# Performance work log

Hardware: AMD Instinct MI355X
Metric: run time of the kernel (lower is better)

## Reference

```python
import jax, jax.numpy as jnp
import numpy as np

# Cyclic permutation matrices applied after each flow step (dimension==3 branch)
P_XY = jnp.array([[0, 1, 0], [1, 0, 0], [0, 0, 1]], dtype=jnp.float32)
P_XZ = jnp.array([[0, 0, 1], [0, 1, 0], [1, 0, 0]], dtype=jnp.float32)
P_YZ = jnp.array([[0, 1, 0], [0, 0, 1], [1, 0, 0]], dtype=jnp.float32)

N = 1_000_000   # number of atoms / samples
FLOW_DEPTH = 8


def setup_inputs() -> dict:
    key = jax.random.key(0)
    k1, k2, k3 = jax.random.split(key, 3)
    z = jax.random.normal(k1, (N, 3), dtype=jnp.float32)
    w = jax.random.normal(k2, (N, FLOW_DEPTH, 3, 3), dtype=jnp.float32)
    b = jax.random.normal(k3, (N, FLOW_DEPTH, 3), dtype=jnp.float32)
    return {"z": z, "w": w, "b": b}


def _flow_zx(z, w, b):
    # z: [N,3], w: [N,D,3,3], b: [N,D,3]
    eye = jnp.eye(3, dtype=w.dtype)
    diag = jnp.diagonal(w, axis1=-2, axis2=-1)               # [N,D,3]
    # LU parameterization: unit lower-tri L, positive diag D, unit upper-tri U
    l = jnp.tril(w, -1) + eye
    u = jnp.triu(w, 1) + eye
    # Faithful to original: log-det uses |0.1 + diag|, D uses |diag| + 0.1
    d_log_det = jnp.sum(jnp.log(jnp.abs(0.1 + diag)), axis=(1, 2))  # [N]
    du = (jnp.abs(diag) + 0.1)[..., :, None] * u             # D @ U, [N,D,3,3]
    W = jnp.einsum('ndij,ndjk->ndik', l, du)                  # L @ D @ U
    perms = [P_XY, P_YZ, P_XZ]
    depth = w.shape[1]
    for idx in range(depth):  # static, small flow depth
        z = jnp.einsum('nb,nbd->nd', z, W[:, idx]) + b[:, idx]
        z = z @ perms[idx % 3]
    return z, d_log_det


def reference(z, w, b):
    return _flow_zx(z, w, b)
```

## Files before the change

### kernel.cpp

```cpp
#include <hip/hip_runtime.h>

#define FLOW_DEPTH 8
#define BLOCK 64
#define W_F4 18
#define B_F4 6

typedef const __attribute__((address_space(1))) void g_void;
typedef __attribute__((address_space(3))) void l_void;

__global__ __launch_bounds__(BLOCK) void graphflow_kernel(
    const float* __restrict__ z_in,
    const float* __restrict__ w,
    const float* __restrict__ b,
    float* __restrict__ out,
    int n_atoms)
{
    __shared__ float4 sw[BLOCK * W_F4];
    __shared__ float4 sb[BLOCK * B_F4];

    const int t = threadIdx.x;
    const int atom0 = blockIdx.x * BLOCK;

    const float4* gw = reinterpret_cast<const float4*>(w) + (size_t)atom0 * W_F4;
    const float4* gb = reinterpret_cast<const float4*>(b) + (size_t)atom0 * B_F4;

    if (atom0 + BLOCK <= n_atoms) {
#pragma unroll
        for (int k = 0; k < W_F4; ++k) {
            __builtin_amdgcn_global_load_lds((g_void*)(gw + k * BLOCK + t),
                                             (l_void*)(sw + k * BLOCK), 16, 0, 0);
        }
#pragma unroll
        for (int k = 0; k < B_F4; ++k) {
            __builtin_amdgcn_global_load_lds((g_void*)(gb + k * BLOCK + t),
                                             (l_void*)(sb + k * BLOCK), 16, 0, 0);
        }
    } else {
        int nw = (n_atoms - atom0) * W_F4;
        for (int k = 0; k < W_F4; ++k) {
            int idx = k * BLOCK + t;
            if (idx < nw) sw[idx] = gw[idx];
        }
        int nb = (n_atoms - atom0) * B_F4;
        for (int k = 0; k < B_F4; ++k) {
            int idx = k * BLOCK + t;
            if (idx < nb) sb[idx] = gb[idx];
        }
    }

    __builtin_amdgcn_s_waitcnt(0);
    __syncthreads();

    const int n = atom0 + t;
    if (n >= n_atoms) return;

    float4 wr[W_F4];
#pragma unroll
    for (int j = 0; j < W_F4; ++j) wr[j] = sw[t * W_F4 + j];
    float4 br[B_F4];
#pragma unroll
    for (int j = 0; j < B_F4; ++j) br[j] = sb[t * B_F4 + j];

    const float* wf = reinterpret_cast<const float*>(wr);
    const float* bf = reinterpret_cast<const float*>(br);

    float z0 = z_in[n * 3 + 0];
    float z1 = z_in[n * 3 + 1];
    float z2 = z_in[n * 3 + 2];

    float logdet = 0.0f;

#pragma unroll
    for (int d = 0; d < FLOW_DEPTH; ++d) {
        const float* W = wf + d * 9;
        float w00 = W[0], w01 = W[1], w02 = W[2];
        float w10 = W[3], w11 = W[4], w12 = W[5];
        float w20 = W[6], w21 = W[7], w22 = W[8];

        float d0 = fabsf(w00) + 0.1f;
        float d1 = fabsf(w11) + 0.1f;
        float d2 = fabsf(w22) + 0.1f;
        logdet += logf(fabsf(0.1f + w00)) +
                  logf(fabsf(0.1f + w11)) +
                  logf(fabsf(0.1f + w22));

        float m01 = d0 * w01;
        float m02 = d0 * w02;
        float m12 = d1 * w12;
        float M00 = d0;
        float M01 = m01;
        float M02 = m02;
        float M10 = w10 * d0;
        float M11 = fmaf(w10, m01, d1);
        float M12 = fmaf(w10, m02, m12);
        float M20 = w20 * d0;
        float M21 = fmaf(w20, m01, w21 * d1);
        float M22 = fmaf(w20, m02, fmaf(w21, m12, d2));

        float t0 = fmaf(z0, M00, fmaf(z1, M10, fmaf(z2, M20, bf[d * 3 + 0])));
        float t1 = fmaf(z0, M01, fmaf(z1, M11, fmaf(z2, M21, bf[d * 3 + 1])));
        float t2 = fmaf(z0, M02, fmaf(z1, M12, fmaf(z2, M22, bf[d * 3 + 2])));

        int p = d % 3;
        if (p == 0) {
            z0 = t1; z1 = t0; z2 = t2;
        } else if (p == 1) {
            z0 = t2; z1 = t0; z2 = t1;
        } else {
            z0 = t2; z1 = t1; z2 = t0;
        }
    }

    out[n * 3 + 0] = z0;
    out[n * 3 + 1] = z1;
    out[n * 3 + 2] = z2;
    out[(size_t)3 * n_atoms + n] = logdet;
}

extern "C" void kernel_launch(void* const* d_in, const int* in_sizes, int n_in,
                              void* d_out, int out_size, void* d_ws, size_t ws_size,
                              hipStream_t stream) {
    const float* z = (const float*)d_in[0];
    const float* w = (const float*)d_in[1];
    const float* b = (const float*)d_in[2];
    float* out = (float*)d_out;

    int n_atoms = in_sizes[0] / 3;
    int grid = (n_atoms + BLOCK - 1) / BLOCK;

    hipLaunchKernelGGL(graphflow_kernel, dim3(grid), dim3(BLOCK), 0, stream,
                       z, w, b, out, n_atoms);
}
```

Before: 447.7 us.

## Pad LDS staging for w, load b directly, fuse log-det logs

Stages w in LDS with one padding float4 per 64 entries so the per-thread strided reads no longer hit the same banks. b is now loaded straight from global into registers, z is loaded before the wait, and the block barrier is dropped on the full-block path. The three logf calls per step are replaced by one fast __logf of the product of the three terms, which trades some accuracy and overflow headroom for fewer transcendental ops. Dropping __syncthreads relies on the wave-sized block (64 threads) so that waitcnt alone orders the LDS writes.

```diff
diff --git a/kernel.cpp b/kernel.cpp
--- a/kernel.cpp
+++ b/kernel.cpp
@@ -4,6 +4,7 @@
 #define BLOCK 64
 #define W_F4 18
 #define B_F4 6
+#define CH   65
 
 typedef const __attribute__((address_space(1))) void g_void;
 typedef __attribute__((address_space(3))) void l_void;
@@ -15,58 +16,54 @@
     float* __restrict__ out,
     int n_atoms)
 {
-    __shared__ float4 sw[BLOCK * W_F4];
-    __shared__ float4 sb[BLOCK * B_F4];
+    __shared__ float4 sw[(W_F4 - 1) * CH + BLOCK];
 
     const int t = threadIdx.x;
     const int atom0 = blockIdx.x * BLOCK;
+    const int n = atom0 + t;
 
     const float4* gw = reinterpret_cast<const float4*>(w) + (size_t)atom0 * W_F4;
-    const float4* gb = reinterpret_cast<const float4*>(b) + (size_t)atom0 * B_F4;
+    const bool full = (atom0 + BLOCK <= n_atoms);
 
-    if (atom0 + BLOCK <= n_atoms) {
+    if (full) {
 #pragma unroll
         for (int k = 0; k < W_F4; ++k) {
             __builtin_amdgcn_global_load_lds((g_void*)(gw + k * BLOCK + t),
-                                             (l_void*)(sw + k * BLOCK), 16, 0, 0);
-        }
-#pragma unroll
-        for (int k = 0; k < B_F4; ++k) {
-            __builtin_amdgcn_global_load_lds((g_void*)(gb + k * BLOCK + t),
-                                             (l_void*)(sb + k * BLOCK), 16, 0, 0);
+                                             (l_void*)(sw + k * CH), 16, 0, 0);
         }
     } else {
         int nw = (n_atoms - atom0) * W_F4;
         for (int k = 0; k < W_F4; ++k) {
             int idx = k * BLOCK + t;
-            if (idx < nw) sw[idx] = gw[idx];
+            if (idx < nw) sw[idx + (idx >> 6)] = gw[idx];
         }
-        int nb = (n_atoms - atom0) * B_F4;
-        for (int k = 0; k < B_F4; ++k) {
-            int idx = k * BLOCK + t;
-            if (idx < nb) sb[idx] = gb[idx];
-        }
+        __syncthreads();
+    }
+
+    float4 br[B_F4];
+    float z0 = 0.f, z1 = 0.f, z2 = 0.f;
+    if (n < n_atoms) {
+        const float4* gb = reinterpret_cast<const float4*>(b) + (size_t)n * B_F4;
+#pragma unroll
+        for (int j = 0; j < B_F4; ++j) br[j] = gb[j];
+        z0 = z_in[n * 3 + 0];
+        z1 = z_in[n * 3 + 1];
+        z2 = z_in[n * 3 + 2];
     }
 
     __builtin_amdgcn_s_waitcnt(0);
-    __syncthreads();
 
-    const int n = atom0 + t;
     if (n >= n_atoms) return;
 
     float4 wr[W_F4];
 #pragma unroll
-    for (int j = 0; j < W_F4; ++j) wr[j] = sw[t * W_F4 + j];
-    float4 br[B_F4];
-#pragma unroll
-    for (int j = 0; j < B_F4; ++j) br[j] = sb[t * B_F4 + j];
+    for (int j = 0; j < W_F4; ++j) {
+        int i = t * W_F4 + j;
+        wr[j] = sw[i + (i >> 6)];
+    }
 
     const float* wf = reinterpret_cast<const float*>(wr);
     const float* bf = reinterpret_cast<const float*>(br);
-
-    float z0 = z_in[n * 3 + 0];
-    float z1 = z_in[n * 3 + 1];
-    float z2 = z_in[n * 3 + 2];
 
     float logdet = 0.0f;
 
@@ -80,9 +77,7 @@
         float d0 = fabsf(w00) + 0.1f;
         float d1 = fabsf(w11) + 0.1f;
         float d2 = fabsf(w22) + 0.1f;
-        logdet += logf(fabsf(0.1f + w00)) +
-                  logf(fabsf(0.1f + w11)) +
-                  logf(fabsf(0.1f + w22));
+        logdet += __logf(fabsf((0.1f + w00) * (0.1f + w11) * (0.1f + w22)));
 
         float m01 = d0 * w01;
         float m02 = d0 * w02;
```

Result: no change. 444.2 us (-0.8%).
